# Kernel optimization log

Hardware: AMD Instinct MI355X
Metric: run time of the kernel (lower is better)

Reference implementation:

```python
import jax, jax.numpy as jnp
import numpy as np

N, K, C, R, S = 10000, 16, 32, 32, 64
D = 9  # per-channel irrep dim of interaction feats: 0e(1)+1o(3)+2e(5)
AVG_NEIGH = 16.0
EPS = 1e-6

_rng = np.random.default_rng(0)
# fixed constant coupling tensors (deterministic stand-ins for CG coefficients; structure matches e3nn paths)
CG112 = jnp.asarray(_rng.standard_normal((3, 3, 5)) * 0.2, jnp.float32)  # 1o x 1o -> 2e
CG121 = jnp.asarray(_rng.standard_normal((3, 5, 3)) * 0.2, jnp.float32)  # 1o x 2e -> 1o
# symmetric tensor-product bases U[order, ir_out]: shape (D,)*order + (mul, ir_dim)
MULS = {3: {'0e': 3, '1o': 2}, 2: {'0e': 2, '1o': 1}, 1: {'0e': 1, '1o': 1}}
IRDIM = {'0e': 1, '1o': 3}
U = {(o, ir): jnp.asarray(_rng.standard_normal((D,) * o + (MULS[o][ir], IRDIM[ir])) * (0.3 ** o), jnp.float32)
     for o in (3, 2, 1) for ir in ('0e', '1o')}


def _normnorm(arrs):
    # E3NormNorm: per-node RMS normalization over channel/component axes
    return [a / jnp.sqrt(jnp.mean(a * a, axis=tuple(range(1, a.ndim)), keepdims=True) + EPS) for a in arrs]


def _sph_harm(vec):
    # real spherical harmonics l=1,2 (component normalization) on normalized vectors
    r = vec / (jnp.linalg.norm(vec, axis=-1, keepdims=True) + EPS)
    x, y, z = r[..., 0], r[..., 1], r[..., 2]
    sh1 = jnp.sqrt(3.0) * r
    c = jnp.sqrt(15.0)
    sh2 = jnp.stack([c * x * y, c * y * z, jnp.sqrt(5.0) / 2 * (3 * z * z - 1), c * x * z, c / 2 * (x * x - y * y)], axis=-1)
    return sh1, sh2


def _forward(node_s, node_v, vectors, radial_embedding, species_table, Wu0, Wu1, radW, radb, ln_g, ln_b,
             Wd0, Wd1, Wd2, w3_0e, w3_1o, w2_0e, w2_1o, w1_0e, w1_1o, P0, P1, Wskip0, Wskip1, Wread,
             receivers, node_specie):
    n, c = node_s.shape
    inv = 1.0 / jnp.sqrt(1.0 * c)
    # ---- InteractionBlock: linear_up + norm ----
    s = node_s @ Wu0 * inv
    v = jnp.einsum('nci,cd->ndi', node_v, Wu1) * inv
    s, v = _normnorm([s, v])
    # ---- MessagePassingConvolution: sender = node i broadcast over its K=16 neighbors ----
    sh1, sh2 = _sph_harm(vectors)  # [n,K,3], [n,K,5]
    m0a = jnp.broadcast_to(s[:, None, :], (n, K, c))                       # prefix 0e
    m0b = jnp.einsum('nci,nki->nkc', v, sh1) / jnp.sqrt(3.0)               # 1o x 1o -> 0e
    m1a = jnp.broadcast_to(v[:, None], (n, K, c, 3))                       # prefix 1o
    m1b = jnp.einsum('nc,nki->nkci', s, sh1) / jnp.sqrt(3.0)               # 0e x 1o -> 1o
    m1c = jnp.einsum('nci,nkp,ipj->nkcj', v, sh2, CG121)                   # 1o x 2e -> 1o
    m2a = jnp.einsum('nc,nkp->nkcp', s, sh2) / jnp.sqrt(5.0)               # 0e x 2e -> 2e
    m2b = jnp.einsum('nci,nkj,ijp->nkcp', v, sh1, CG112)                   # 1o x 1o -> 2e
    M0 = jnp.concatenate([m0a, m0b], axis=-1)      # [n,K,2C]
    M1 = jnp.concatenate([m1a, m1b, m1c], axis=2)  # [n,K,3C,3]
    M2 = jnp.concatenate([m2a, m2b], axis=2)       # [n,K,2C,5]
    # radial mix: linear + layernorm, one weight per irrep (7C total)
    rad = radial_embedding @ radW + radb
    mu = rad.mean(-1, keepdims=True)
    var = rad.var(-1, keepdims=True)
    rad = ln_g * (rad - mu) / jnp.sqrt(var + EPS) + ln_b
    r0, r1, r2 = rad[..., :2 * c], rad[..., 2 * c:5 * c], rad[..., 5 * c:]
    M0 = M0 * r0
    M1 = M1 * r1[..., None]
    M2 = M2 * r2[..., None]
    # scatter-add messages to receivers, normalize by sqrt(avg_num_neighbors)
    idx = receivers.reshape(-1)
    sc = 1.0 / jnp.sqrt(AVG_NEIGH)
    o0 = jnp.zeros((n, 2 * c), M0.dtype).at[idx].add(M0.reshape(n * K, 2 * c)) * sc
    o1 = jnp.zeros((n, 3 * c, 3), M1.dtype).at[idx].add(M1.reshape(n * K, 3 * c, 3)) * sc
    o2 = jnp.zeros((n, 2 * c, 5), M2.dtype).at[idx].add(M2.reshape(n * K, 2 * c, 5)) * sc
    o0, o1, o2 = _normnorm([o0, o1, o2])
    # linear_down to interaction_irreps Cx(0e+1o+2e), then norm
    A0 = o0 @ Wd0 / jnp.sqrt(2.0 * c)
    A1 = jnp.einsum('nmi,md->ndi', o1, Wd1) / jnp.sqrt(3.0 * c)
    A2 = jnp.einsum('nmi,md->ndi', o2, Wd2) / jnp.sqrt(2.0 * c)
    A0, A1, A2 = _normnorm([A0, A1, A2])
    # ---- EquivariantProductBasisBlock: species-gathered symmetric contraction ----
    x_sym = jnp.concatenate([A0[:, :, None], A1, A2], axis=-1)  # [n, C, D=9]
    species_ind = species_table[node_specie]                    # [n, R]
    Wsym = {(3, '0e'): w3_0e, (3, '1o'): w3_1o, (2, '0e'): w2_0e, (2, '1o'): w2_1o, (1, '0e'): w1_0e, (1, '1o'): w1_1o}
    out = {}
    for order in (3, 2, 1):
        for ir in ('0e', '1o'):
            u = U[(order, ir)]
            w = jnp.einsum('be,ekc->bkc', species_ind, Wsym[(order, ir)])
            if ir not in out:
                out[ir] = ('new', jnp.einsum('...jki,bkc,bcj->bc...i', u, w, x_sym))
            else:
                out[ir] = out[ir] + jnp.einsum('...ki,bkc->bc...i', u, w)
        for ir in ('0e', '1o'):
            if isinstance(out[ir], tuple):
                out[ir] = out[ir][1]  # creation order already consumed one x
            else:
                out[ir] = jnp.einsum('bc...ji,bcj->bc...i', out[ir], x_sym)
    sym_s = out['0e'][..., 0]  # [n, C]
    sym_v = out['1o']          # [n, C, 3]
    # proj_out linear
    ps = sym_s @ P0 * inv
    pv = jnp.einsum('nci,cd->ndi', sym_v, P1) * inv
    # species-indexed skip connection
    skip_s = jnp.einsum('nc,ncd->nd', node_s, Wskip0[node_specie]) * inv
    skip_v = jnp.einsum('nci,ncd->ndi', node_v, Wskip1[node_specie]) * inv
    s_out = ps + skip_s
    v_out = pv + skip_v
    # linear readout (output_irreps = 1x0e)
    read = s_out @ Wread * inv
    return jnp.concatenate([s_out, v_out.reshape(n, 3 * c), read], axis=-1)


def setup_inputs():
    ks = jax.random.split(jax.random.key(0), 32)
    f = lambda i, shape: jax.random.normal(ks[i], shape, jnp.float32)
    return {
        'node_s': f(0, (N, C)),
        'node_v': f(1, (N, C, 3)),
        'vectors': f(2, (N, K, 3)),
        'radial_embedding': f(3, (N, K, R)),
        'receivers': jax.random.randint(ks[4], (N, K), 0, N),
        'node_specie': jax.random.randint(ks[5], (N,), 0, S),
        'species_table': f(6, (S, R)),
        'Wu0': f(7, (C, C)), 'Wu1': f(8, (C, C)),
        'radW': f(9, (R, 7 * C)), 'radb': jnp.zeros((7 * C,), jnp.float32),
        'ln_g': jnp.ones((7 * C,), jnp.float32), 'ln_b': jnp.zeros((7 * C,), jnp.float32),
        'Wd0': f(11, (2 * C, C)), 'Wd1': f(12, (3 * C, C)), 'Wd2': f(13, (2 * C, C)),
        'w3_0e': f(14, (R, 3, C)), 'w3_1o': f(15, (R, 2, C)),
        'w2_0e': f(16, (R, 2, C)), 'w2_1o': f(17, (R, 1, C)),
        'w1_0e': f(18, (R, 1, C)), 'w1_1o': f(19, (R, 1, C)),
        'P0': f(20, (C, C)), 'P1': f(21, (C, C)),
        'Wskip0': f(22, (S, C, C)), 'Wskip1': f(23, (S, C, C)),
        'Wread': f(24, (C, 1)),
    }


def reference(node_s, node_v, vectors, radial_embedding, receivers, node_specie, species_table, Wu0, Wu1,
              radW, radb, ln_g, ln_b, Wd0, Wd1, Wd2, w3_0e, w3_1o, w2_0e, w2_1o, w1_0e, w1_1o,
              P0, P1, Wskip0, Wskip1, Wread):
    return _forward(node_s, node_v, vectors, radial_embedding, species_table, Wu0, Wu1, radW, radb, ln_g, ln_b,
                    Wd0, Wd1, Wd2, w3_0e, w3_1o, w2_0e, w2_1o, w1_0e, w1_1o, P0, P1, Wskip0, Wskip1, Wread,
                    receivers, node_specie)
```

## Files before the change

kernel.cpp:

```cpp
#include <hip/hip_runtime.h>
#include <cmath>
#include <stdint.h>

typedef unsigned long long u64;
typedef unsigned __int128 u128;

#define EPSF 1e-6f

#define OFF_RAW 0L
#define OFF_S   7168L
#define OFF_G   8960L
#define GSP_SZ  28032L
#define OFF_SN  (OFF_G + 64L*GSP_SZ)
#define OFF_VN  (OFF_SN + 320000L)
#define FLOAT_END (OFF_VN + 960000L)
#define OFF_RAD (FLOAT_END + 262144L)
#define RAD_REQ_BYTES ((size_t)(OFF_RAD + 35840000L) * 4)

#define IOFF_DEG   0
#define IOFF_OFFS  10000
#define IOFF_CUR   20001
#define IOFF_EL    30001
#define IOFF_SCNT  190001
#define IOFF_SOFF  190065
#define IOFF_SCUR  190130
#define IOFF_NORD  190194
#define IOFF_TRI   200194
#define IOFF_PAIR  200359


__device__ __forceinline__ u128 pcg_mul128() {
  return ((u128)2549297995355413924ULL << 64) | (u128)4865540595714422341ULL;
}
struct Pcg {
  u128 state, inc;
  __device__ __forceinline__ u64 next() {
    state = state * pcg_mul128() + inc;
    u64 hi = (u64)(state >> 64), lo = (u64)state;
    unsigned rot = (unsigned)(hi >> 58);
    u64 x = hi ^ lo;
    return (x >> rot) | (x << ((64u - rot) & 63u));
  }
};
__device__ __forceinline__ double u64_to_dbl(u64 u) {
  return (double)(u >> 11) * (1.0 / 9007199254740992.0);
}
__device__ __forceinline__ unsigned ss_hashmix(unsigned v, unsigned &hc) {
  v ^= hc; hc *= 0x931e8875u; v *= hc; v ^= v >> 16; return v;
}
__device__ __forceinline__ unsigned ss_mix(unsigned x, unsigned y) {
  unsigned r = 0xca01f9ddu * x - 0x4973f715u * y; r ^= r >> 16; return r;
}

#define NBUF 8192
#define NBM  8191
#define PERTH 32
#define NDRAW 7092
#define NSEG  222

__global__ __launch_bounds__(256) void k_constants(float* __restrict__ wsf, int* __restrict__ wsi)
{
  __shared__ double wi[256], fi[256];
  __shared__ u64 ki[256];
  __shared__ u64 buf[NBUF];
  __shared__ float zv[NBUF];
  __shared__ unsigned char cons[NBUF];
  __shared__ unsigned short jmp[NBUF];
  __shared__ unsigned short heads[NSEG];
  __shared__ u64 sseed[4];
  __shared__ u64 stst[512], enst[512];
  __shared__ double scl[8];
  __shared__ int flag;
  const int tid = threadIdx.x;
  float* raw = wsf + OFF_RAW;

  if (tid == 0) {
    flag = 0;
    unsigned hc = 0x43b0d7e5u;
    unsigned pool[4];
    for (int i = 0; i < 4; i++) pool[i] = ss_hashmix(0u, hc);
    for (int s = 0; s < 4; s++)
      for (int d = 0; d < 4; d++)
        if (s != d) pool[d] = ss_mix(pool[d], ss_hashmix(pool[s], hc));
    unsigned hb = 0x8b51f9ddu;
    u64 sw[4];
    {
      unsigned w8[8];
      for (int i = 0; i < 8; i++) {
        unsigned dv = pool[i & 3];
        dv ^= hb; hb *= 0x58f38dedu; dv *= hb; dv ^= dv >> 16;
        w8[i] = dv;
      }
      for (int k2 = 0; k2 < 4; k2++) sw[k2] = (u64)w8[2*k2] | ((u64)w8[2*k2+1] << 32);
    }
    u128 initstate = ((u128)sw[0] << 64) | (u128)sw[1];
    u128 initseq   = ((u128)sw[2] << 64) | (u128)sw[3];
    u128 inc_ = (initseq << 1) | (u128)1;
    u128 S0 = inc_;
    S0 += initstate;
    S0 = S0 * pcg_mul128() + inc_;
    sseed[0] = (u64)(S0 >> 64);   sseed[1] = (u64)S0;
    sseed[2] = (u64)(inc_ >> 64); sseed[3] = (u64)inc_;
    double p2 = pow(0.3, 2.0), p3 = pow(0.3, 3.0);
    scl[0]=0.2; scl[1]=0.2; scl[2]=p3; scl[3]=p3; scl[4]=p2; scl[5]=p2; scl[6]=0.3; scl[7]=0.3;
    const double m1 = 4503599627370496.0;
    const double ZR = 3.6541528853610087963519472518;
    double dn = ZR, tn = ZR;
    const double vn = 4.92867323399e-3;
    double fv = exp(-0.5 * dn * dn);
    double q = vn / fv;
    ki[0] = (u64)((dn / q) * m1);
    ki[1] = 0;
    wi[0] = q / m1;  wi[255] = dn / m1;
    fi[0] = 1.0;     fi[255] = fv;
    for (int i = 254; i >= 1; i--) {
      dn = sqrt(-2.0 * log(vn / dn + fv));
      ki[i+1] = (u64)((dn / tn) * m1);
      tn = dn;
      fv = exp(-0.5 * dn * dn);
      fi[i] = fv;
      wi[i] = dn / m1;
    }
    int mcnt = 0;
    for (int a = 0; a < 9; a++)
      for (int b = a; b < 9; b++)
        for (int j3 = b; j3 < 9; j3++)
          wsi[IOFF_TRI + (mcnt++)] = a | (b << 4) | (j3 << 8);
    int pcnt = 0;
    for (int a = 0; a < 9; a++)
      for (int b = a; b < 9; b++)
        wsi[IOFF_PAIR + (pcnt++)] = a | (b << 4);
  }
  __syncthreads();

  {
    u128 S0   = ((u128)sseed[0] << 64) | (u128)sseed[1];
    u128 inc_ = ((u128)sseed[2] << 64) | (u128)sseed[3];
    u128 aR = (u128)1, cR = (u128)0;
    u128 aP = pcg_mul128(), cP = inc_;
    unsigned e = (unsigned)tid * PERTH;
    while (e) {
      if (e & 1u) { cR = aP * cR + cP; aR = aP * aR; }
      cP = aP * cP + cP;
      aP = aP * aP;
      e >>= 1;
    }
    Pcg g; g.inc = inc_; g.state = aR * S0 + cR;
    stst[tid*2] = (u64)(g.state >> 64); stst[tid*2+1] = (u64)g.state;
    #pragma unroll 4
    for (int k = 0; k < PERTH; k++) buf[tid*PERTH + k] = g.next();
    enst[tid*2] = (u64)(g.state >> 64); enst[tid*2+1] = (u64)g.state;
  }
  __syncthreads();
  if (tid < 255) {
    if (stst[(tid+1)*2] != enst[tid*2] || stst[(tid+1)*2+1] != enst[tid*2+1])
      atomicOr(&flag, 1);
  }
  if (tid == 0) {
    if (fabs(u64_to_dbl(buf[0]) - 0.6369616873214543) > 1e-12) atomicOr(&flag, 1);
  }
  __syncthreads();
  if (flag && tid == 0) {
    u128 S0   = ((u128)sseed[0] << 64) | (u128)sseed[1];
    u128 inc_ = ((u128)sseed[2] << 64) | (u128)sseed[3];
    Pcg g; g.state = S0; g.inc = inc_;
    for (int k = 0; k < NBUF; k++) buf[k] = g.next();
  }
  __syncthreads();

  const double ZRd  = 3.6541528853610087963519472518;
  const double ZIRd = 0.27366123732975827203338247596;
  for (int k = 0; k < PERTH; k++) {
    const int p = tid*PERTH + k;
    int pos = p;
    int consumed = 0;
    double z = 0.0;
    u64 r = buf[pos & NBM]; pos++; consumed++;
    for (int guard = 0; guard < 64; guard++) {
      int idx = (int)(r & 0xff);
      r >>= 8;
      int sgn = (int)(r & 1);
      u64 rabs = (r >> 1) & 0x000fffffffffffffULL;
      double x = (double)rabs * wi[idx];
      if (sgn) x = -x;
      if (rabs < ki[idx]) { z = x; break; }
      if (idx == 0) {
        double xx = 0.0, yy = 0.0;
        for (int g2 = 0; g2 < 64; g2++) {
          u64 ua = buf[pos & NBM]; pos++; consumed++;
          u64 ub = buf[pos & NBM]; pos++; consumed++;
          xx = -ZIRd * log1p(-u64_to_dbl(ua));
          yy = -log1p(-u64_to_dbl(ub));
          if (yy + yy > xx * xx) break;
        }
        z = ((rabs >> 8) & 1) ? -(ZRd + xx) : (ZRd + xx);
        break;
      } else {
        u64 u = buf[pos & NBM]; pos++; consumed++;
        if ((fi[idx-1] - fi[idx]) * u64_to_dbl(u) + fi[idx] < exp(-0.5 * x * x)) { z = x; break; }
      }
      r = buf[pos & NBM]; pos++; consumed++;
    }
    zv[p] = (float)z;
    cons[p] = (unsigned char)(consumed > 255 ? 255 : consumed);
  }
  __syncthreads();

  {
    int pos[PERTH];
    #pragma unroll
    for (int k = 0; k < PERTH; k++) pos[k] = tid*PERTH + k;
    for (int s = 0; s < 32; s++) {
      #pragma unroll
      for (int k = 0; k < PERTH; k++) {
        int np = pos[k] + (int)cons[pos[k]];
        pos[k] = (np > NBM) ? NBM : np;
      }
    }
    #pragma unroll
    for (int k = 0; k < PERTH; k++) jmp[tid*PERTH + k] = (unsigned short)pos[k];
  }
  __syncthreads();

  if (tid == 0) {
    int pos = 0;
    for (int m = 0; m < NSEG; m++) { heads[m] = (unsigned short)pos; pos = (int)jmp[pos]; }
  }
  __syncthreads();

  if (tid < NSEG) {
    int pos = (int)heads[tid];
    const int i0 = tid * 32;
    for (int k = 0; k < 32; k++) {
      const int i = i0 + k;
      if (i >= NDRAW) break;
      double sc;
      if      (i < 90)   sc = scl[0];
      else if (i < 6651) sc = scl[2];
      else if (i < 7056) sc = scl[4];
      else               sc = scl[6];
      raw[i] = (float)((double)zv[pos] * sc);
      int np = pos + (int)cons[pos];
      pos = (np > NBM) ? NBM : np;
    }
  }
  __syncthreads();

  float* Sb = wsf + OFF_S;
  for (int idx = tid; idx < 495; idx += 256) {
    int m = idx / 3, k2 = idx % 3;
    int tp = wsi[IOFF_TRI + m];
    int a = tp & 15, b = (tp >> 4) & 15, j3 = (tp >> 8) & 15;
    int P[6][3] = {{a,b,j3},{a,j3,b},{b,a,j3},{b,j3,a},{j3,a,b},{j3,b,a}};
    float s = 0.f;
    for (int t = 0; t < 6; t++) {
      bool dup = false;
      for (int u = 0; u < t; u++)
        if (P[u][0]==P[t][0] && P[u][1]==P[t][1] && P[u][2]==P[t][2]) { dup = true; break; }
      if (!dup) s += raw[90 + ((P[t][0]*9 + P[t][1])*9 + P[t][2])*3 + k2];
    }
    Sb[m*3 + k2] = s;
  }
  for (int idx = tid; idx < 990; idx += 256) {
    int m = idx / 6, r6 = idx % 6, k2 = r6 / 3, i = r6 % 3;
    int tp = wsi[IOFF_TRI + m];
    int a = tp & 15, b = (tp >> 4) & 15, j3 = (tp >> 8) & 15;
    int P[6][3] = {{a,b,j3},{a,j3,b},{b,a,j3},{b,j3,a},{j3,a,b},{j3,b,a}};
    float s = 0.f;
    for (int t = 0; t < 6; t++) {
      bool dup = false;
      for (int u = 0; u < t; u++)
        if (P[u][0]==P[t][0] && P[u][1]==P[t][1] && P[u][2]==P[t][2]) { dup = true; break; }
      if (!dup) s += raw[2277 + (((P[t][0]*9 + P[t][1])*9 + P[t][2])*2 + k2)*3 + i];
    }
    Sb[495 + (m*2 + k2)*3 + i] = s;
  }
  for (int idx = tid; idx < 90; idx += 256) {
    int m = idx / 2, k2 = idx % 2;
    int pp = wsi[IOFF_PAIR + m]; int a = pp & 15, b = (pp >> 4) & 15;
    float s = raw[6651 + (a*9 + b)*2 + k2];
    if (a != b) s += raw[6651 + (b*9 + a)*2 + k2];
    Sb[1485 + idx] = s;
  }
  for (int idx = tid; idx < 135; idx += 256) {
    int m = idx / 3, i = idx % 3;
    int pp = wsi[IOFF_PAIR + m]; int a = pp & 15, b = (pp >> 4) & 15;
    float s = raw[6813 + (a*9 + b)*3 + i];
    if (a != b) s += raw[6813 + (b*9 + a)*3 + i];
    Sb[1575 + idx] = s;
  }
  for (int idx = tid; idx < 9;  idx += 256) Sb[1710 + idx] = raw[7056 + idx];
  for (int idx = tid; idx < 27; idx += 256) Sb[1719 + idx] = raw[7065 + idx];
}

#define RB_E 32
__global__ __launch_bounds__(256) void k_prep(
    const float* __restrict__ ns, const float* __restrict__ nv,
    const float* __restrict__ Wu0, const float* __restrict__ Wu1,
    const float* __restrict__ remb, const float* __restrict__ radW,
    const float* __restrict__ radb, const float* __restrict__ ln_g,
    const float* __restrict__ ln_b,
    const int* __restrict__ recv, const int* __restrict__ spec,
    int doRad,
    float* __restrict__ wsf, int* __restrict__ wsi)
{
  __shared__ __align__(16) float shbuf[8672];
  const int tid = threadIdx.x;
  const int bid = blockIdx.x;

  if (bid < 1250) {
    const int nn = bid * 8 + (tid >> 5);
    const int c = tid & 31;
    const float INV = 0.17677669529663687f;
    float s = 0.f;
    for (int e = 0; e < 32; e++) s += ns[nn*32 + e] * Wu0[e*32 + c];
    s *= INV;
    float v0 = 0, v1 = 0, v2 = 0;
    for (int e = 0; e < 32; e++) {
      const float w = Wu1[e*32 + c];
      const float* p = nv + (long)(nn*32 + e)*3;
      v0 += p[0]*w; v1 += p[1]*w; v2 += p[2]*w;
    }
    v0 *= INV; v1 *= INV; v2 *= INV;
    float ss = s*s;
    for (int m = 16; m >= 1; m >>= 1) ss += __shfl_xor(ss, m);
    float sv = v0*v0 + v1*v1 + v2*v2;
    for (int m = 16; m >= 1; m >>= 1) sv += __shfl_xor(sv, m);
    float rs = rsqrtf(ss * (1.f/32.f) + EPSF);
    float rv = rsqrtf(sv * (1.f/96.f) + EPSF);
    wsf[OFF_SN + nn*32 + c] = s * rs;
    float* vp = wsf + OFF_VN + (long)(nn*32 + c)*3;
    vp[0] = v0*rv; vp[1] = v1*rv; vp[2] = v2*rv;
  } else if (bid < 6250) {
    if (!doRad) return;
    float (*er)[33] = (float(*)[33])&shbuf[0];
    float* pre = &shbuf[1056];
    float4* lg4 = (float4*)&shbuf[8224];
    float4* lb4 = (float4*)&shbuf[8448];
    const long e0 = (long)(bid - 1250) * RB_E;

    if (tid < 56) { lg4[tid] = ((const float4*)ln_g)[tid]; lb4[tid] = ((const float4*)ln_b)[tid]; }
    for (int i = tid; i < RB_E*32; i += 256) {
      const int e = i >> 5, q = i & 31;
      er[e][q] = remb[(e0 + e)*32 + q];
    }
    __syncthreads();

    if (tid < 224) {
      const int cg = tid % 56, grp = tid / 56;
      const float4 rb = ((const float4*)radb)[cg];
      float4 acc[8];
      #pragma unroll
      for (int k = 0; k < 8; k++) acc[k] = rb;
      const float4* radW4 = (const float4*)radW;
      for (int q = 0; q < 32; q++) {
        const float4 w = radW4[q*56 + cg];
        #pragma unroll
        for (int k = 0; k < 8; k++) {
          const float ev = er[grp*8 + k][q];
          acc[k].x = fmaf(ev, w.x, acc[k].x);
          acc[k].y = fmaf(ev, w.y, acc[k].y);
          acc[k].z = fmaf(ev, w.z, acc[k].z);
          acc[k].w = fmaf(ev, w.w, acc[k].w);
        }
      }
      #pragma unroll
      for (int k = 0; k < 8; k++)
        ((float4*)&pre[(grp*8 + k)*224])[cg] = acc[k];
    }
    __syncthreads();

    const int wv = tid >> 6, ln = tid & 63;
    for (int k = 0; k < 8; k++) {
      const int e = wv*8 + k;
      float a0 = 0.f, a1 = 0.f, a2 = 0.f, a3 = 0.f;
      if (ln < 56) {
        const float4 v = ((const float4*)&pre[e*224])[ln];
        a0 = v.x; a1 = v.y; a2 = v.z; a3 = v.w;
      }
      float c1 = a0 + a1 + a2 + a3;
      float c2 = a0*a0 + a1*a1 + a2*a2 + a3*a3;
      for (int m = 32; m >= 1; m >>= 1) { c1 += __shfl_xor(c1, m); c2 += __shfl_xor(c2, m); }
      const float mu = c1 * (1.f/224.f);
      const float rvar = rsqrtf(c2*(1.f/224.f) - mu*mu + EPSF);
      if (ln < 56) {
        const float4 lg = lg4[ln], lb = lb4[ln];
        float4 o;
        o.x = lg.x*(a0-mu)*rvar + lb.x;
        o.y = lg.y*(a1-mu)*rvar + lb.y;
        o.z = lg.z*(a2-mu)*rvar + lb.z;
        o.w = lg.w*(a3-mu)*rvar + lb.w;
        ((float4*)(wsf + OFF_RAD))[(e0 + e)*56 + ln] = o;
      }
    }
  } else {
    const int e = (bid - 6250)*256 + tid;
    if (e < 160000) atomicAdd(&wsi[IOFF_DEG + recv[e]], 1);
    if (e < 10000)  atomicAdd(&wsi[IOFF_SCNT + spec[e]], 1);
  }
}

__global__ __launch_bounds__(1024) void k_scan(int* __restrict__ wsi) {
  __shared__ int part[1024];
  const int tid = threadIdx.x;
  int loc[10];
  int base = tid * 10;
  int s = 0;
  for (int t = 0; t < 10; t++) {
    int idx = base + t;
    loc[t] = s;
    s += (idx < 10000) ? wsi[IOFF_DEG + idx] : 0;
  }
  part[tid] = s;
  __syncthreads();
  for (int d = 1; d < 1024; d <<= 1) {
    int v = (tid >= d) ? part[tid - d] : 0;
    __syncthreads();
    part[tid] += v;
    __syncthreads();
  }
  int exc = (tid > 0) ? part[tid - 1] : 0;
  for (int t = 0; t < 10; t++) {
    int idx = base + t;
    if (idx <= 10000) wsi[IOFF_OFFS + idx] = exc + loc[t];
  }
  if (tid == 0) {
    int a = 0;
    for (int s2 = 0; s2 < 64; s2++) { wsi[IOFF_SOFF + s2] = a; a += wsi[IOFF_SCNT + s2]; }
    wsi[IOFF_SOFF + 64] = a;
  }
}

__global__ __launch_bounds__(256) void k_fillg(
    const int* __restrict__ recv, const int* __restrict__ spec,
    const float* __restrict__ stab,
    const float* __restrict__ w30e, const float* __restrict__ w31o,
    const float* __restrict__ w20e, const float* __restrict__ w21o,
    const float* __restrict__ w10e, const float* __restrict__ w11o,
    float* __restrict__ wsf, int* __restrict__ wsi)
{
  __shared__ float st[32];
  const int tid = threadIdx.x;
  const int bid = blockIdx.x;
  if (bid < 625) {
    const int e = bid*256 + tid;
    if (e < 160000) {
      int r = recv[e];
      int p = atomicAdd(&wsi[IOFF_CUR + r], 1);
      wsi[IOFF_EL + wsi[IOFF_OFFS + r] + p] = e;
    }
    if (e < 10000) {
      int sp = spec[e];
      int p = atomicAdd(&wsi[IOFF_SCUR + sp], 1);
      wsi[IOFF_NORD + wsi[IOFF_SOFF + sp] + p] = e;
    }
  } else {
    const int sp = bid - 625;
    float* Gsp = wsf + OFF_G + (long)sp * GSP_SZ;
    if (tid < 32) st[tid] = stab[sp*32 + tid];
    __syncthreads();
    for (int t = tid; t < 320; t += 256) {
      const float* W; int kc, kcs;
      if (t < 96)       { W = w30e; kc = t;       kcs = 96; }
      else if (t < 160) { W = w31o; kc = t - 96;  kcs = 64; }
      else if (t < 224) { W = w20e; kc = t - 160; kcs = 64; }
      else if (t < 256) { W = w21o; kc = t - 224; kcs = 32; }
      else if (t < 288) { W = w10e; kc = t - 256; kcs = 32; }
      else              { W = w11o; kc = t - 288; kcs = 32; }
      float a = 0.f;
      for (int e = 0; e < 32; e++) a += st[e] * W[e*kcs + kc];
      Gsp[t] = a;
    }
  }
}

__device__ __forceinline__ float msg_fast(int slot,
    const float* __restrict__ se, const float* __restrict__ ve,
    const float* __restrict__ sh, const float* __restrict__ ab,
    const float* __restrict__ rd)
{
  const float IS3 = 0.57735026918962576f;
  const float IS5 = 0.44721359549995794f;
  float val; int radidx;
  if (slot < 64) {
    radidx = slot;
    if (slot < 32) val = se[slot];
    else {
      int c = slot - 32;
      val = (ve[c*3+0]*sh[0] + ve[c*3+1]*sh[1] + ve[c*3+2]*sh[2]) * IS3;
    }
  } else if (slot < 352) {
    int q = slot - 64; int row = q / 3; int i = q - row*3;
    radidx = 64 + row;
    if (row < 32) val = ve[row*3 + i];
    else if (row < 64) val = se[row - 32] * sh[i] * IS3;
    else {
      int c = row - 64;
      val = ve[c*3+0]*ab[0+i] + ve[c*3+1]*ab[3+i] + ve[c*3+2]*ab[6+i];
    }
  } else {
    int q = slot - 352; int row = q / 5; int p = q - row*5;
    radidx = 160 + row;
    if (row < 32) val = se[row] * sh[3+p] * IS5;
    else {
      int c = row - 32;
      val = ve[c*3+0]*ab[9+p] + ve[c*3+1]*ab[14+p] + ve[c*3+2]*ab[19+p];
    }
  }
  return val * rd[radidx];
}

#define SM_RAD 0
#define SM_SE  896
#define SM_VE  1024
#define SM_ER  1408
#define SM_SHH 1536
#define SM_AB  1568
#define SM_LNG 1664
#define SM_LNB 1888
#define SM_RB  2112
#define SM_CG  2336
#define SM_S    0
#define SM_X    1746
#define SM_O    2034
#define SM_GRED 2706
#define SM_SYMS 3730
#define SM_SYMV 3762
#define SM_SOUT 3858
#define SM_REDB 3890
#define SM_RF   3902
#define SMEM_N  3906

template<int PRE>
__global__ __launch_bounds__(256) void k_main(
    const float* __restrict__ node_s, const float* __restrict__ node_v,
    const float* __restrict__ vectors, const float* __restrict__ remb,
    const int* __restrict__ nspec,
    const float* __restrict__ radW, const float* __restrict__ radb,
    const float* __restrict__ ln_g, const float* __restrict__ ln_b,
    const float* __restrict__ Wd0, const float* __restrict__ Wd1, const float* __restrict__ Wd2,
    const float* __restrict__ P0, const float* __restrict__ P1,
    const float* __restrict__ Wsk0, const float* __restrict__ Wsk1,
    const float* __restrict__ Wread,
    const float* __restrict__ wsf, const int* __restrict__ wsi,
    float* __restrict__ out)
{
  const int tid = threadIdx.x;
  const int wv  = tid >> 6;
  const int ln  = tid & 63;
  __shared__ __align__(16) float smem[SMEM_N];
  __shared__ int tri_s[165], pair_s[45];

  const int j  = wsi[IOFF_NORD + blockIdx.x];
  const int sp = nspec[j];
  const int e0 = wsi[IOFF_OFFS + j];
  const int e1 = wsi[IOFF_OFFS + j + 1];

  if (!PRE) {
    for (int i = tid; i < 224; i += 256) {
      smem[SM_LNG + i] = ln_g[i];
      smem[SM_LNB + i] = ln_b[i];
      smem[SM_RB  + i] = radb[i];
    }
  }
  for (int i = tid; i < 90; i += 256) smem[SM_CG + i] = wsf[OFF_RAW + i];
  __syncthreads();

  float acc0 = 0.f, acc1 = 0.f, acc2 = 0.f;
  for (int t = e0; t < e1; t += 4) {
    const int eidx = t + wv;
    const bool act = (eidx < e1);
    if (act) {
      const int e = wsi[IOFF_EL + eidx];
      const int n = e >> 4;
      if (ln < 32) {
        smem[SM_SE + wv*32 + ln] = wsf[OFF_SN + (long)n*32 + ln];
        if (!PRE) smem[SM_ER + wv*32 + ln] = remb[(long)e*32 + ln];
      } else {
        const int l2 = ln - 32;
        const float* vp = wsf + OFF_VN + (long)(n*32 + l2)*3;
        smem[SM_VE + wv*96 + l2*3+0] = vp[0];
        smem[SM_VE + wv*96 + l2*3+1] = vp[1];
        smem[SM_VE + wv*96 + l2*3+2] = vp[2];
      }
      if (ln == 0) {
        const float* vv = vectors + (long)e*3;
        float vx = vv[0], vy = vv[1], vz = vv[2];
        float nr = sqrtf(vx*vx + vy*vy + vz*vz) + EPSF;
        float rx = vx/nr, ry = vy/nr, rz = vz/nr;
        smem[SM_SHH + wv*8 + 0] = 1.7320508075688772f * rx;
        smem[SM_SHH + wv*8 + 1] = 1.7320508075688772f * ry;
        smem[SM_SHH + wv*8 + 2] = 1.7320508075688772f * rz;
        smem[SM_SHH + wv*8 + 3] = 3.872983346207417f * rx*ry;
        smem[SM_SHH + wv*8 + 4] = 3.872983346207417f * ry*rz;
        smem[SM_SHH + wv*8 + 5] = 1.118033988749895f * (3.f*rz*rz - 1.f);
        smem[SM_SHH + wv*8 + 6] = 3.872983346207417f * rx*rz;
        smem[SM_SHH + wv*8 + 7] = 1.9364916731037085f * (rx*rx - ry*ry);
      }
      if (PRE) {
        if (ln < 56) {
          const float4 v4 = ((const float4*)(wsf + OFF_RAD))[(long)e*56 + ln];
          ((float4*)&smem[SM_RAD + wv*224])[ln] = v4;
        }
      } else {
        float aval[4];
        float c1 = 0.f, c2 = 0.f;
        #pragma unroll
        for (int k = 0; k < 4; k++) {
          const int ch = ln + 64*k;
          if (ch < 224) {
            float a = smem[SM_RB + ch];
            #pragma unroll 8
            for (int q = 0; q < 32; q++)
              a += smem[SM_ER + wv*32 + q] * radW[q*224 + ch];
            aval[k] = a; c1 += a; c2 += a*a;
          }
        }
        for (int m = 32; m >= 1; m >>= 1) { c1 += __shfl_xor(c1, m); c2 += __shfl_xor(c2, m); }
        const float mu = c1 * (1.f/224.f);
        const float rvar = rsqrtf(c2*(1.f/224.f) - mu*mu + EPSF);
        #pragma unroll
        for (int k = 0; k < 4; k++) {
          const int ch = ln + 64*k;
          if (ch < 224)
            smem[SM_RAD + wv*224 + ch] = smem[SM_LNG + ch]*(aval[k]-mu)*rvar + smem[SM_LNB + ch];
// ... 78 lines not shown
  if (tid < 32) {
    int q = tid + 128, d = q/5, p = q - d*5;
    float a = 0;
    for (int m = 0; m < 64; m++) a += o_lds[352 + m*5 + p] * Wd2[m*32 + d];
    av2 = a * 0.125f;
  }
  float p0 = (tid < 32) ? av1*av1 : 0.f;
  float p1 = (tid >= 32 && tid < 128) ? av1*av1 : 0.f;
  float p2s = (tid >= 128) ? av1*av1 : 0.f;
  if (tid < 32) p2s += av2*av2;
  for (int m = 32; m >= 1; m >>= 1) { p0 += __shfl_xor(p0, m); p1 += __shfl_xor(p1, m); p2s += __shfl_xor(p2s, m); }
  if ((tid & 63) == 0) { redbuf[wv] = p0; redbuf[4+wv] = p1; redbuf[8+wv] = p2s; }
  __syncthreads();
  if (tid == 0) {
    float s0 = redbuf[0]+redbuf[1]+redbuf[2]+redbuf[3];
    float s1 = redbuf[4]+redbuf[5]+redbuf[6]+redbuf[7];
    float s2 = redbuf[8]+redbuf[9]+redbuf[10]+redbuf[11];
    rf[0] = rsqrtf(s0*(1.f/32.f)  + EPSF);
    rf[1] = rsqrtf(s1*(1.f/96.f)  + EPSF);
    rf[2] = rsqrtf(s2*(1.f/160.f) + EPSF);
  }
  __syncthreads();
  float* x_lds = &smem[SM_X];
  if (tid < 32) x_lds[tid*9 + 0] = av1 * rf[0];
  else if (tid < 128) { int q = tid - 32, d = q/3, i = q - d*3; x_lds[d*9 + 1 + i] = av1 * rf[1]; }
  else { int q = tid - 128, d = q/5, p = q - d*5; x_lds[d*9 + 4 + p] = av1 * rf[2]; }
  if (tid < 32) { int q = tid + 128, d = q/5, p = q - d*5; x_lds[d*9 + 4 + p] = av2 * rf[2]; }
  __syncthreads();

  const float* Sb = &smem[SM_S];
  float* gred = &smem[SM_GRED];
  const int c = tid & 31, g = tid >> 5;
  float xr[9];
  for (int t2 = 0; t2 < 9; t2++) xr[t2] = x_lds[c*9 + t2];
  const float* wl = wsf + OFF_G + (long)sp * GSP_SZ;
  const float w30a = wl[c], w30b = wl[32 + c], w30c = wl[64 + c];
  const float w31a = wl[96 + c], w31b = wl[128 + c];
  const float w20a = wl[160 + c], w20b = wl[192 + c];
  const float w21  = wl[224 + c];
  const float w10  = wl[256 + c];
  const float w11  = wl[288 + c];

  float sa = 0, va0 = 0, va1 = 0, va2 = 0;
  for (int m = g; m < 165; m += 8) {
    const int tp = tri_s[m];
    const float P = xr[tp & 15] * xr[(tp >> 4) & 15] * xr[(tp >> 8) & 15];
    sa += P * (Sb[m*3+0]*w30a + Sb[m*3+1]*w30b + Sb[m*3+2]*w30c);
    const float* s1p = &Sb[495 + m*6];
    va0 += P * (s1p[0]*w31a + s1p[3]*w31b);
    va1 += P * (s1p[1]*w31a + s1p[4]*w31b);
    va2 += P * (s1p[2]*w31a + s1p[5]*w31b);
  }
  for (int m = g; m < 45; m += 8) {
    const int pp = pair_s[m];
    const float P = xr[pp & 15] * xr[(pp >> 4) & 15];
    sa += P * (Sb[1485 + m*2+0]*w20a + Sb[1485 + m*2+1]*w20b);
    const float* s1p = &Sb[1575 + m*3];
    va0 += P * s1p[0] * w21;
    va1 += P * s1p[1] * w21;
    va2 += P * s1p[2] * w21;
  }
  if (g == 0) {
    for (int a = 0; a < 9; a++) {
      const float xa = xr[a];
      sa += xa * Sb[1710 + a] * w10;
      va0 += xa * Sb[1719 + a*3 + 0] * w11;
      va1 += xa * Sb[1719 + a*3 + 1] * w11;
      va2 += xa * Sb[1719 + a*3 + 2] * w11;
    }
  }
  gred[0*256 + g*32 + c] = sa;
  gred[1*256 + g*32 + c] = va0;
  gred[2*256 + g*32 + c] = va1;
  gred[3*256 + g*32 + c] = va2;
  __syncthreads();
  float* syms = &smem[SM_SYMS];
  float* symv = &smem[SM_SYMV];
  float* sout = &smem[SM_SOUT];
  if (tid < 128) {
    int cc = tid & 31, comp = tid >> 5;
    float a = 0;
    for (int gg = 0; gg < 8; gg++) a += gred[comp*256 + gg*32 + cc];
    if (comp == 0) syms[cc] = a; else symv[cc*3 + comp - 1] = a;
  }
  __syncthreads();

  const float INV = 0.17677669529663687f;
  if (tid < 32) {
    int d = tid; float ps = 0, sk = 0;
    const float* Wp = Wsk0 + (long)sp * 1024;
    for (int c2 = 0; c2 < 32; c2++) {
      ps += syms[c2] * P0[c2*32 + d];
      sk += node_s[j*32 + c2] * Wp[c2*32 + d];
    }
    float val = (ps + sk) * INV;
    sout[d] = val;
    out[(long)j*129 + d] = val;
  } else if (tid < 128) {
    int q = tid - 32, d = q/3, i = q - d*3;
    float pv = 0, sk = 0;
    const float* Wp = Wsk1 + (long)sp * 1024;
    for (int c2 = 0; c2 < 32; c2++) {
      pv += symv[c2*3 + i] * P1[c2*32 + d];
      sk += node_v[(long)(j*32 + c2)*3 + i] * Wp[c2*32 + d];
    }
    out[(long)j*129 + 32 + q] = (pv + sk) * INV;
  }
  __syncthreads();
  if (tid < 32) {
    float p = sout[tid] * Wread[tid];
    for (int m = 16; m >= 1; m >>= 1) p += __shfl_xor(p, m);
    if (tid == 0) out[(long)j*129 + 128] = p * INV;
  }
}

extern "C" void kernel_launch(void* const* d_in, const int* in_sizes, int n_in,
                              void* d_out, int out_size, void* d_ws, size_t ws_size,
                              hipStream_t stream)
{
  const float* node_s  = (const float*)d_in[0];
  const float* node_v  = (const float*)d_in[1];
  const float* vectors = (const float*)d_in[2];
  const float* remb    = (const float*)d_in[3];
  const int*   recv    = (const int*)d_in[4];
  const int*   nspec   = (const int*)d_in[5];
  const float* stab    = (const float*)d_in[6];
  const float* Wu0     = (const float*)d_in[7];
  const float* Wu1     = (const float*)d_in[8];
  const float* radW    = (const float*)d_in[9];
  const float* radb    = (const float*)d_in[10];
  const float* ln_g    = (const float*)d_in[11];
  const float* ln_b    = (const float*)d_in[12];
  const float* Wd0     = (const float*)d_in[13];
  const float* Wd1     = (const float*)d_in[14];
  const float* Wd2     = (const float*)d_in[15];
  const float* w30e    = (const float*)d_in[16];
  const float* w31o    = (const float*)d_in[17];
  const float* w20e    = (const float*)d_in[18];
  const float* w21o    = (const float*)d_in[19];
  const float* w10e    = (const float*)d_in[20];
  const float* w11o    = (const float*)d_in[21];
  const float* P0      = (const float*)d_in[22];
  const float* P1      = (const float*)d_in[23];
  const float* Wsk0    = (const float*)d_in[24];
  const float* Wsk1    = (const float*)d_in[25];
  const float* Wread   = (const float*)d_in[26];
  float* out = (float*)d_out;
  float* wsf = (float*)d_ws;
  int*   wsi = (int*)((char*)d_ws + FLOAT_END * sizeof(float));

  const bool pre = (ws_size >= RAD_REQ_BYTES);

  hipMemsetAsync(wsi, 0, (size_t)IOFF_NORD * sizeof(int), stream);
  k_constants<<<1, 256, 0, stream>>>(wsf, wsi);
  k_prep<<<6875, 256, 0, stream>>>(node_s, node_v, Wu0, Wu1,
                                   remb, radW, radb, ln_g, ln_b,
                                   recv, nspec, pre ? 1 : 0, wsf, wsi);
  k_scan<<<1, 1024, 0, stream>>>(wsi);
  k_fillg<<<689, 256, 0, stream>>>(recv, nspec, stab,
                                   w30e, w31o, w20e, w21o, w10e, w11o,
                                   wsf, wsi);
  if (pre) {
    k_main<1><<<10000, 256, 0, stream>>>(node_s, node_v, vectors, remb, nspec,
                                         radW, radb, ln_g, ln_b, Wd0, Wd1, Wd2,
                                         P0, P1, Wsk0, Wsk1, Wread, wsf, wsi, out);
  } else {
    k_main<0><<<10000, 256, 0, stream>>>(node_s, node_v, vectors, remb, nspec,
                                         radW, radb, ln_g, ln_b, Wd0, Wd1, Wd2,
                                         P0, P1, Wsk0, Wsk1, Wread, wsf, wsi, out);
  }
}
```

Measured before the change: 632.7 us.

## Fold constant generation into prep, scan, and fillg kernels to cut serial launches

```diff
diff --git a/kernel.cpp b/kernel.cpp
--- a/kernel.cpp
+++ b/kernel.cpp
@@ -16,6 +16,7 @@
 #define FLOAT_END (OFF_VN + 960000L)
 #define OFF_RAD (FLOAT_END + 262144L)
 #define RAD_REQ_BYTES ((size_t)(OFF_RAD + 35840000L) * 4)
+#define OFF_RNG (OFF_G + 8192L)
 
 #define IOFF_DEG   0
 #define IOFF_OFFS  10000
@@ -57,25 +58,117 @@
 #define PERTH 32
 #define NDRAW 7092
 #define NSEG  222
-
-__global__ __launch_bounds__(256) void k_constants(float* __restrict__ wsf, int* __restrict__ wsi)
+#define RB_E 32
+
+__global__ __launch_bounds__(256) void k_prep(
+    const float* __restrict__ ns, const float* __restrict__ nv,
+    const float* __restrict__ Wu0, const float* __restrict__ Wu1,
+    const float* __restrict__ remb, const float* __restrict__ radW,
+    const float* __restrict__ radb, const float* __restrict__ ln_g,
+    const float* __restrict__ ln_b,
+    const int* __restrict__ recv, const int* __restrict__ spec,
+    int doRad,
+    float* __restrict__ wsf, int* __restrict__ wsi)
 {
-  __shared__ double wi[256], fi[256];
-  __shared__ u64 ki[256];
-  __shared__ u64 buf[NBUF];
-  __shared__ float zv[NBUF];
-  __shared__ unsigned char cons[NBUF];
-  __shared__ unsigned short jmp[NBUF];
-  __shared__ unsigned short heads[NSEG];
-  __shared__ u64 sseed[4];
-  __shared__ u64 stst[512], enst[512];
-  __shared__ double scl[8];
-  __shared__ int flag;
+  __shared__ __align__(16) float shbuf[8672];
   const int tid = threadIdx.x;
-  float* raw = wsf + OFF_RAW;
-
-  if (tid == 0) {
-    flag = 0;
+  const int bid = blockIdx.x;
+
+  if (bid < 1250) {
+    const int nn = bid * 8 + (tid >> 5);
+    const int c = tid & 31;
+    const float INV = 0.17677669529663687f;
+    float s = 0.f;
+    for (int e = 0; e < 32; e++) s += ns[nn*32 + e] * Wu0[e*32 + c];
+    s *= INV;
+    float v0 = 0, v1 = 0, v2 = 0;
+    for (int e = 0; e < 32; e++) {
+      const float w = Wu1[e*32 + c];
+      const float* p = nv + (long)(nn*32 + e)*3;
+      v0 += p[0]*w; v1 += p[1]*w; v2 += p[2]*w;
+    }
+    v0 *= INV; v1 *= INV; v2 *= INV;
+    float ss = s*s;
+    for (int m = 16; m >= 1; m >>= 1) ss += __shfl_xor(ss, m);
+    float sv = v0*v0 + v1*v1 + v2*v2;
+    for (int m = 16; m >= 1; m >>= 1) sv += __shfl_xor(sv, m);
+    float rs = rsqrtf(ss * (1.f/32.f) + EPSF);
+    float rv = rsqrtf(sv * (1.f/96.f) + EPSF);
+    wsf[OFF_SN + nn*32 + c] = s * rs;
+    float* vp = wsf + OFF_VN + (long)(nn*32 + c)*3;
+    vp[0] = v0*rv; vp[1] = v1*rv; vp[2] = v2*rv;
+  } else if (bid < 6250) {
+    if (!doRad) return;
+    float (*er)[33] = (float(*)[33])&shbuf[0];
+    float* pre = &shbuf[1056];
+    float4* lg4 = (float4*)&shbuf[8224];
+    float4* lb4 = (float4*)&shbuf[8448];
+    const long e0 = (long)(bid - 1250) * RB_E;
+
+    if (tid < 56) { lg4[tid] = ((const float4*)ln_g)[tid]; lb4[tid] = ((const float4*)ln_b)[tid]; }
+    for (int i = tid; i < RB_E*32; i += 256) {
+      const int e = i >> 5, q = i & 31;
+      er[e][q] = remb[(e0 + e)*32 + q];
+    }
+    __syncthreads();
+
+    if (tid < 224) {
+      const int cg = tid % 56, grp = tid / 56;
+      const float4 rb = ((const float4*)radb)[cg];
+      float4 acc[8];
+      #pragma unroll
+      for (int k = 0; k < 8; k++) acc[k] = rb;
+      const float4* radW4 = (const float4*)radW;
+      for (int q = 0; q < 32; q++) {
+        const float4 w = radW4[q*56 + cg];
+        #pragma unroll
+        for (int k = 0; k < 8; k++) {
+          const float ev = er[grp*8 + k][q];
+          acc[k].x = fmaf(ev, w.x, acc[k].x);
+          acc[k].y = fmaf(ev, w.y, acc[k].y);
+          acc[k].z = fmaf(ev, w.z, acc[k].z);
+          acc[k].w = fmaf(ev, w.w, acc[k].w);
+        }
+      }
+      #pragma unroll
+      for (int k = 0; k < 8; k++)
+        ((float4*)&pre[(grp*8 + k)*224])[cg] = acc[k];
+    }
+    __syncthreads();
+
+    const int wv = tid >> 6, ln = tid & 63;
+    for (int k = 0; k < 8; k++) {
+      const int e = wv*8 + k;
+      float a0 = 0.f, a1 = 0.f, a2 = 0.f, a3 = 0.f;
+      if (ln < 56) {
+        const float4 v = ((const float4*)&pre[e*224])[ln];
+        a0 = v.x; a1 = v.y; a2 = v.z; a3 = v.w;
+      }
+      float c1 = a0 + a1 + a2 + a3;
+      float c2 = a0*a0 + a1*a1 + a2*a2 + a3*a3;
+      for (int m = 32; m >= 1; m >>= 1) { c1 += __shfl_xor(c1, m); c2 += __shfl_xor(c2, m); }
+      const float mu = c1 * (1.f/224.f);
+      const float rvar = rsqrtf(c2*(1.f/224.f) - mu*mu + EPSF);
+      if (ln < 56) {
+        const float4 lg = lg4[ln], lb = lb4[ln];
+        float4 o;
+        o.x = lg.x*(a0-mu)*rvar + lb.x;
+        o.y = lg.y*(a1-mu)*rvar + lb.y;
+        o.z = lg.z*(a2-mu)*rvar + lb.z;
+        o.w = lg.w*(a3-mu)*rvar + lb.w;
+        ((float4*)(wsf + OFF_RAD))[(e0 + e)*56 + ln] = o;
+      }
+    }
+  } else if (bid < 6875) {
+    const int e = (bid - 6250)*256 + tid;
+    if (e < 160000) atomicAdd(&wsi[IOFF_DEG + recv[e]], 1);
+    if (e < 10000)  atomicAdd(&wsi[IOFF_SCNT + spec[e]], 1);
+  } else {
+    if (tid != 0) return;
+    double* wiG = (double*)(wsf + OFF_RNG);
+    double* fiG = (double*)(wsf + OFF_RNG + 512);
+    u64*    kiG = (u64*)   (wsf + OFF_RNG + 1024);
+    u64*    ssG = (u64*)   (wsf + OFF_RNG + 1536);
     unsigned hc = 0x43b0d7e5u;
     unsigned pool[4];
     for (int i = 0; i < 4; i++) pool[i] = ss_hashmix(0u, hc);
@@ -99,27 +192,25 @@
     u128 S0 = inc_;
     S0 += initstate;
     S0 = S0 * pcg_mul128() + inc_;
-    sseed[0] = (u64)(S0 >> 64);   sseed[1] = (u64)S0;
-    sseed[2] = (u64)(inc_ >> 64); sseed[3] = (u64)inc_;
-    double p2 = pow(0.3, 2.0), p3 = pow(0.3, 3.0);
-    scl[0]=0.2; scl[1]=0.2; scl[2]=p3; scl[3]=p3; scl[4]=p2; scl[5]=p2; scl[6]=0.3; scl[7]=0.3;
+    ssG[0] = (u64)(S0 >> 64);   ssG[1] = (u64)S0;
+    ssG[2] = (u64)(inc_ >> 64); ssG[3] = (u64)inc_;
     const double m1 = 4503599627370496.0;
     const double ZR = 3.6541528853610087963519472518;
     double dn = ZR, tn = ZR;
     const double vn = 4.92867323399e-3;
     double fv = exp(-0.5 * dn * dn);
     double q = vn / fv;
-    ki[0] = (u64)((dn / q) * m1);
-    ki[1] = 0;
-    wi[0] = q / m1;  wi[255] = dn / m1;
-    fi[0] = 1.0;     fi[255] = fv;
+    kiG[0] = (u64)((dn / q) * m1);
+    kiG[1] = 0;
+    wiG[0] = q / m1;  wiG[255] = dn / m1;
+    fiG[0] = 1.0;     fiG[255] = fv;
     for (int i = 254; i >= 1; i--) {
       dn = sqrt(-2.0 * log(vn / dn + fv));
-      ki[i+1] = (u64)((dn / tn) * m1);
+      kiG[i+1] = (u64)((dn / tn) * m1);
       tn = dn;
       fv = exp(-0.5 * dn * dn);
-      fi[i] = fv;
-      wi[i] = dn / m1;
+      fiG[i] = fv;
+      wiG[i] = dn / m1;
     }
     int mcnt = 0;
     for (int a = 0; a < 9; a++)
@@ -131,11 +222,70 @@
       for (int b = a; b < 9; b++)
         wsi[IOFF_PAIR + (pcnt++)] = a | (b << 4);
   }
+}
+
+__global__ __launch_bounds__(256) void k_mid(float* __restrict__ wsf, int* __restrict__ wsi)
+{
+  __shared__ double wi[256], fi[256];
+  __shared__ u64 ki[256];
+  __shared__ u64 buf[NBUF];
+  __shared__ float zv[NBUF];
+  __shared__ unsigned char cons[NBUF];
+  __shared__ unsigned short jmp[NBUF];
+  __shared__ unsigned short heads[NSEG];
+  __shared__ u64 stst[512], enst[512];
+  __shared__ double scl[8];
+  __shared__ int flag;
+  __shared__ int part[256];
+  const int tid = threadIdx.x;
+
+  if (blockIdx.x == 1) {
+    int loc[40];
+    const int base = tid * 40;
+    int s = 0;
+    for (int t = 0; t < 40; t++) {
+      const int idx = base + t;
+      loc[t] = s;
+      s += (idx < 10000) ? wsi[IOFF_DEG + idx] : 0;
+    }
+    part[tid] = s;
+    __syncthreads();
+    for (int d = 1; d < 256; d <<= 1) {
+      int v = (tid >= d) ? part[tid - d] : 0;
+      __syncthreads();
+      part[tid] += v;
+      __syncthreads();
+    }
+    const int exc = (tid > 0) ? part[tid - 1] : 0;
+    for (int t = 0; t < 40; t++) {
+      const int idx = base + t;
+      if (idx <= 10000) wsi[IOFF_OFFS + idx] = exc + loc[t];
+    }
+    if (tid == 0) {
+      int a = 0;
+      for (int s2 = 0; s2 < 64; s2++) { wsi[IOFF_SOFF + s2] = a; a += wsi[IOFF_SCNT + s2]; }
+      wsi[IOFF_SOFF + 64] = a;
+    }
+    return;
+  }
+
+  const double* wiG = (const double*)(wsf + OFF_RNG);
+  const double* fiG = (const double*)(wsf + OFF_RNG + 512);
+  const u64*    kiG = (const u64*)   (wsf + OFF_RNG + 1024);
+  const u64*    ssG = (const u64*)   (wsf + OFF_RNG + 1536);
+  float* raw = wsf + OFF_RAW;
+
+  wi[tid] = wiG[tid]; fi[tid] = fiG[tid]; ki[tid] = kiG[tid];
+  if (tid == 0) {
+    flag = 0;
+    double p2 = pow(0.3, 2.0), p3 = pow(0.3, 3.0);
+    scl[0]=0.2; scl[1]=0.2; scl[2]=p3; scl[3]=p3; scl[4]=p2; scl[5]=p2; scl[6]=0.3; scl[7]=0.3;
+  }
   __syncthreads();
 
   {
-    u128 S0   = ((u128)sseed[0] << 64) | (u128)sseed[1];
-    u128 inc_ = ((u128)sseed[2] << 64) | (u128)sseed[3];
+    u128 S0   = ((u128)ssG[0] << 64) | (u128)ssG[1];
+    u128 inc_ = ((u128)ssG[2] << 64) | (u128)ssG[3];
     u128 aR = (u128)1, cR = (u128)0;
     u128 aP = pcg_mul128(), cP = inc_;
     unsigned e = (unsigned)tid * PERTH;
@@ -161,8 +311,8 @@
   }
   __syncthreads();
   if (flag && tid == 0) {
-    u128 S0   = ((u128)sseed[0] << 64) | (u128)sseed[1];
-    u128 inc_ = ((u128)sseed[2] << 64) | (u128)sseed[3];
+    u128 S0   = ((u128)ssG[0] << 64) | (u128)ssG[1];
+    u128 inc_ = ((u128)ssG[2] << 64) | (u128)ssG[3];
     Pcg g; g.state = S0; g.inc = inc_;
     for (int k = 0; k < NBUF; k++) buf[k] = g.next();
   }
@@ -244,191 +394,6 @@
       pos = (np > NBM) ? NBM : np;
     }
   }
-  __syncthreads();
-
-  float* Sb = wsf + OFF_S;
-  for (int idx = tid; idx < 495; idx += 256) {
-    int m = idx / 3, k2 = idx % 3;
-    int tp = wsi[IOFF_TRI + m];
-    int a = tp & 15, b = (tp >> 4) & 15, j3 = (tp >> 8) & 15;
-    int P[6][3] = {{a,b,j3},{a,j3,b},{b,a,j3},{b,j3,a},{j3,a,b},{j3,b,a}};
-    float s = 0.f;
-    for (int t = 0; t < 6; t++) {
-      bool dup = false;
-      for (int u = 0; u < t; u++)
-        if (P[u][0]==P[t][0] && P[u][1]==P[t][1] && P[u][2]==P[t][2]) { dup = true; break; }
-      if (!dup) s += raw[90 + ((P[t][0]*9 + P[t][1])*9 + P[t][2])*3 + k2];
-    }
-    Sb[m*3 + k2] = s;
-  }
-  for (int idx = tid; idx < 990; idx += 256) {
-    int m = idx / 6, r6 = idx % 6, k2 = r6 / 3, i = r6 % 3;
-    int tp = wsi[IOFF_TRI + m];
-    int a = tp & 15, b = (tp >> 4) & 15, j3 = (tp >> 8) & 15;
-    int P[6][3] = {{a,b,j3},{a,j3,b},{b,a,j3},{b,j3,a},{j3,a,b},{j3,b,a}};
-    float s = 0.f;
-    for (int t = 0; t < 6; t++) {
-      bool dup = false;
-      for (int u = 0; u < t; u++)
-        if (P[u][0]==P[t][0] && P[u][1]==P[t][1] && P[u][2]==P[t][2]) { dup = true; break; }
-      if (!dup) s += raw[2277 + (((P[t][0]*9 + P[t][1])*9 + P[t][2])*2 + k2)*3 + i];
-    }
-    Sb[495 + (m*2 + k2)*3 + i] = s;
-  }
-  for (int idx = tid; idx < 90; idx += 256) {
-    int m = idx / 2, k2 = idx % 2;
-    int pp = wsi[IOFF_PAIR + m]; int a = pp & 15, b = (pp >> 4) & 15;
-    float s = raw[6651 + (a*9 + b)*2 + k2];
-    if (a != b) s += raw[6651 + (b*9 + a)*2 + k2];
-    Sb[1485 + idx] = s;
-  }
-  for (int idx = tid; idx < 135; idx += 256) {
-    int m = idx / 3, i = idx % 3;
-    int pp = wsi[IOFF_PAIR + m]; int a = pp & 15, b = (pp >> 4) & 15;
-    float s = raw[6813 + (a*9 + b)*3 + i];
-    if (a != b) s += raw[6813 + (b*9 + a)*3 + i];
-    Sb[1575 + idx] = s;
-  }
-  for (int idx = tid; idx < 9;  idx += 256) Sb[1710 + idx] = raw[7056 + idx];
-  for (int idx = tid; idx < 27; idx += 256) Sb[1719 + idx] = raw[7065 + idx];
-}
-
-#define RB_E 32
-__global__ __launch_bounds__(256) void k_prep(
-    const float* __restrict__ ns, const float* __restrict__ nv,
-    const float* __restrict__ Wu0, const float* __restrict__ Wu1,
-    const float* __restrict__ remb, const float* __restrict__ radW,
-    const float* __restrict__ radb, const float* __restrict__ ln_g,
-    const float* __restrict__ ln_b,
-    const int* __restrict__ recv, const int* __restrict__ spec,
-    int doRad,
-    float* __restrict__ wsf, int* __restrict__ wsi)
-{
-  __shared__ __align__(16) float shbuf[8672];
-  const int tid = threadIdx.x;
-  const int bid = blockIdx.x;
-
-  if (bid < 1250) {
-    const int nn = bid * 8 + (tid >> 5);
-    const int c = tid & 31;
-    const float INV = 0.17677669529663687f;
-    float s = 0.f;
-    for (int e = 0; e < 32; e++) s += ns[nn*32 + e] * Wu0[e*32 + c];
-    s *= INV;
-    float v0 = 0, v1 = 0, v2 = 0;
-    for (int e = 0; e < 32; e++) {
-      const float w = Wu1[e*32 + c];
-      const float* p = nv + (long)(nn*32 + e)*3;
-      v0 += p[0]*w; v1 += p[1]*w; v2 += p[2]*w;
-    }
-    v0 *= INV; v1 *= INV; v2 *= INV;
-    float ss = s*s;
-    for (int m = 16; m >= 1; m >>= 1) ss += __shfl_xor(ss, m);
-    float sv = v0*v0 + v1*v1 + v2*v2;
-    for (int m = 16; m >= 1; m >>= 1) sv += __shfl_xor(sv, m);
-    float rs = rsqrtf(ss * (1.f/32.f) + EPSF);
-    float rv = rsqrtf(sv * (1.f/96.f) + EPSF);
-    wsf[OFF_SN + nn*32 + c] = s * rs;
-    float* vp = wsf + OFF_VN + (long)(nn*32 + c)*3;
-    vp[0] = v0*rv; vp[1] = v1*rv; vp[2] = v2*rv;
-  } else if (bid < 6250) {
-    if (!doRad) return;
-    float (*er)[33] = (float(*)[33])&shbuf[0];
-    float* pre = &shbuf[1056];
-    float4* lg4 = (float4*)&shbuf[8224];
-    float4* lb4 = (float4*)&shbuf[8448];
-    const long e0 = (long)(bid - 1250) * RB_E;
-
-    if (tid < 56) { lg4[tid] = ((const float4*)ln_g)[tid]; lb4[tid] = ((const float4*)ln_b)[tid]; }
-    for (int i = tid; i < RB_E*32; i += 256) {
-      const int e = i >> 5, q = i & 31;
-      er[e][q] = remb[(e0 + e)*32 + q];
-    }
-    __syncthreads();
-
-    if (tid < 224) {
-      const int cg = tid % 56, grp = tid / 56;
-      const float4 rb = ((const float4*)radb)[cg];
-      float4 acc[8];
-      #pragma unroll
-      for (int k = 0; k < 8; k++) acc[k] = rb;
-      const float4* radW4 = (const float4*)radW;
-      for (int q = 0; q < 32; q++) {
-        const float4 w = radW4[q*56 + cg];
-        #pragma unroll
-        for (int k = 0; k < 8; k++) {
-          const float ev = er[grp*8 + k][q];
-          acc[k].x = fmaf(ev, w.x, acc[k].x);
-          acc[k].y = fmaf(ev, w.y, acc[k].y);
-          acc[k].z = fmaf(ev, w.z, acc[k].z);
-          acc[k].w = fmaf(ev, w.w, acc[k].w);
-        }
-      }
-      #pragma unroll
-      for (int k = 0; k < 8; k++)
-        ((float4*)&pre[(grp*8 + k)*224])[cg] = acc[k];
-    }
-    __syncthreads();
-
-    const int wv = tid >> 6, ln = tid & 63;
-    for (int k = 0; k < 8; k++) {
-      const int e = wv*8 + k;
-      float a0 = 0.f, a1 = 0.f, a2 = 0.f, a3 = 0.f;
-      if (ln < 56) {
-        const float4 v = ((const float4*)&pre[e*224])[ln];
-        a0 = v.x; a1 = v.y; a2 = v.z; a3 = v.w;
-      }
-      float c1 = a0 + a1 + a2 + a3;
-      float c2 = a0*a0 + a1*a1 + a2*a2 + a3*a3;
-      for (int m = 32; m >= 1; m >>= 1) { c1 += __shfl_xor(c1, m); c2 += __shfl_xor(c2, m); }
-      const float mu = c1 * (1.f/224.f);
-      const float rvar = rsqrtf(c2*(1.f/224.f) - mu*mu + EPSF);
-      if (ln < 56) {
-        const float4 lg = lg4[ln], lb = lb4[ln];
-        float4 o;
-        o.x = lg.x*(a0-mu)*rvar + lb.x;
-        o.y = lg.y*(a1-mu)*rvar + lb.y;
-        o.z = lg.z*(a2-mu)*rvar + lb.z;
-        o.w = lg.w*(a3-mu)*rvar + lb.w;
-        ((float4*)(wsf + OFF_RAD))[(e0 + e)*56 + ln] = o;
-      }
-    }
-  } else {
-    const int e = (bid - 6250)*256 + tid;
-    if (e < 160000) atomicAdd(&wsi[IOFF_DEG + recv[e]], 1);
-    if (e < 10000)  atomicAdd(&wsi[IOFF_SCNT + spec[e]], 1);
-  }
-}
-
-__global__ __launch_bounds__(1024) void k_scan(int* __restrict__ wsi) {
-  __shared__ int part[1024];
-  const int tid = threadIdx.x;
-  int loc[10];
-  int base = tid * 10;
-  int s = 0;
-  for (int t = 0; t < 10; t++) {
-    int idx = base + t;
-    loc[t] = s;
-    s += (idx < 10000) ? wsi[IOFF_DEG + idx] : 0;
-  }
-  part[tid] = s;
-  __syncthreads();
-  for (int d = 1; d < 1024; d <<= 1) {
-    int v = (tid >= d) ? part[tid - d] : 0;
-    __syncthreads();
-    part[tid] += v;
-    __syncthreads();
-  }
-  int exc = (tid > 0) ? part[tid - 1] : 0;
-  for (int t = 0; t < 10; t++) {
-    int idx = base + t;
-    if (idx <= 10000) wsi[IOFF_OFFS + idx] = exc + loc[t];
-  }
-  if (tid == 0) {
-    int a = 0;
-    for (int s2 = 0; s2 < 64; s2++) { wsi[IOFF_SOFF + s2] = a; a += wsi[IOFF_SCNT + s2]; }
-    wsi[IOFF_SOFF + 64] = a;
-  }
 }
 
 __global__ __launch_bounds__(256) void k_fillg(
@@ -454,7 +419,7 @@
       int p = atomicAdd(&wsi[IOFF_SCUR + sp], 1);
       wsi[IOFF_NORD + wsi[IOFF_SOFF + sp] + p] = e;
     }
-  } else {
+  } else if (bid < 689) {
     const int sp = bid - 625;
     float* Gsp = wsf + OFF_G + (long)sp * GSP_SZ;
     if (tid < 32) st[tid] = stab[sp*32 + tid];
@@ -471,6 +436,53 @@
       for (int e = 0; e < 32; e++) a += st[e] * W[e*kcs + kc];
       Gsp[t] = a;
     }
+  } else {
+    const float* raw = wsf + OFF_RAW;
+    float* Sb = wsf + OFF_S;
+    for (int idx = tid; idx < 495; idx += 256) {
+      int m = idx / 3, k2 = idx % 3;
+      int tp = wsi[IOFF_TRI + m];
+      int a = tp & 15, b = (tp >> 4) & 15, j3 = (tp >> 8) & 15;
+      int P[6][3] = {{a,b,j3},{a,j3,b},{b,a,j3},{b,j3,a},{j3,a,b},{j3,b,a}};
+      float s = 0.f;
+      for (int t = 0; t < 6; t++) {
+        bool dup = false;
+        for (int u = 0; u < t; u++)
+          if (P[u][0]==P[t][0] && P[u][1]==P[t][1] && P[u][2]==P[t][2]) { dup = true; break; }
+        if (!dup) s += raw[90 + ((P[t][0]*9 + P[t][1])*9 + P[t][2])*3 + k2];
+      }
+      Sb[m*3 + k2] = s;
+    }
+    for (int idx = tid; idx < 990; idx += 256) {
+      int m = idx / 6, r6 = idx % 6, k2 = r6 / 3, i = r6 % 3;
+      int tp = wsi[IOFF_TRI + m];
+      int a = tp & 15, b = (tp >> 4) & 15, j3 = (tp >> 8) & 15;
+      int P[6][3] = {{a,b,j3},{a,j3,b},{b,a,j3},{b,j3,a},{j3,a,b},{j3,b,a}};
+      float s = 0.f;
+      for (int t = 0; t < 6; t++) {
+        bool dup = false;
+        for (int u = 0; u < t; u++)
+          if (P[u][0]==P[t][0] && P[u][1]==P[t][1] && P[u][2]==P[t][2]) { dup = true; break; }
+        if (!dup) s += raw[2277 + (((P[t][0]*9 + P[t][1])*9 + P[t][2])*2 + k2)*3 + i];
+      }
+      Sb[495 + (m*2 + k2)*3 + i] = s;
+    }
+    for (int idx = tid; idx < 90; idx += 256) {
+      int m = idx / 2, k2 = idx % 2;
+      int pp = wsi[IOFF_PAIR + m]; int a = pp & 15, b = (pp >> 4) & 15;
+      float s = raw[6651 + (a*9 + b)*2 + k2];
+      if (a != b) s += raw[6651 + (b*9 + a)*2 + k2];
+      Sb[1485 + idx] = s;
+    }
+    for (int idx = tid; idx < 135; idx += 256) {
+      int m = idx / 3, i = idx % 3;
+      int pp = wsi[IOFF_PAIR + m]; int a = pp & 15, b = (pp >> 4) & 15;
+      float s = raw[6813 + (a*9 + b)*3 + i];
+      if (a != b) s += raw[6813 + (b*9 + a)*3 + i];
+      Sb[1575 + idx] = s;
+    }
+    for (int idx = tid; idx < 9;  idx += 256) Sb[1710 + idx] = raw[7056 + idx];
+    for (int idx = tid; idx < 27; idx += 256) Sb[1719 + idx] = raw[7065 + idx];
   }
 }
 
@@ -855,12 +867,11 @@
   const bool pre = (ws_size >= RAD_REQ_BYTES);
 
   hipMemsetAsync(wsi, 0, (size_t)IOFF_NORD * sizeof(int), stream);
-  k_constants<<<1, 256, 0, stream>>>(wsf, wsi);
-  k_prep<<<6875, 256, 0, stream>>>(node_s, node_v, Wu0, Wu1,
+  k_prep<<<6876, 256, 0, stream>>>(node_s, node_v, Wu0, Wu1,
                                    remb, radW, radb, ln_g, ln_b,
                                    recv, nspec, pre ? 1 : 0, wsf, wsi);
-  k_scan<<<1, 1024, 0, stream>>>(wsi);
-  k_fillg<<<689, 256, 0, stream>>>(recv, nspec, stab,
+  k_mid<<<2, 256, 0, stream>>>(wsf, wsi);
+  k_fillg<<<690, 256, 0, stream>>>(recv, nspec, stab,
                                    w30e, w31o, w20e, w21o, w10e, w11o,
                                    wsf, wsi);
   if (pre) {
```

Result: faster. 596.9 us (-5.7%).
